# Kernel optimization log

Hardware: AMD Instinct MI355X
Metric: run time of the kernel (lower is better)

Reference implementation:

```python
import jax, jax.numpy as jnp
import numpy as np

N = 20000      # nodes
E = 160000     # edges (avg degree 16)
IN_DIM = 256
HID = 128      # hidden_dim == per-head out_channels in PyG TransformerConv
HEADS = 4
EPS = 1e-5


def setup_inputs() -> dict:
    key = jax.random.key(0)
    ks = jax.random.split(key, 24)

    def w(k, shape, scale=0.05):
        return jax.random.normal(k, shape, dtype=jnp.float32) * scale

    inp = {
        "x": jax.random.normal(ks[0], (N, IN_DIM), dtype=jnp.float32),
        "edge_index": jax.random.randint(ks[1], (2, E), 0, N, dtype=jnp.int32),
        # input projection
        "lin_w": w(ks[2], (IN_DIM, HID)), "lin_b": jnp.zeros((HID,), jnp.float32),
    }
    i = 3
    for l in (1, 2):
        inp[f"q_w{l}"] = w(ks[i], (HID, HEADS * HID)); i += 1
        inp[f"q_b{l}"] = jnp.zeros((HEADS * HID,), jnp.float32)
        inp[f"k_w{l}"] = w(ks[i], (HID, HEADS * HID)); i += 1
        inp[f"k_b{l}"] = jnp.zeros((HEADS * HID,), jnp.float32)
        inp[f"v_w{l}"] = w(ks[i], (HID, HEADS * HID)); i += 1
        inp[f"v_b{l}"] = jnp.zeros((HEADS * HID,), jnp.float32)
        inp[f"s_w{l}"] = w(ks[i], (HID, HID)); i += 1
        inp[f"s_b{l}"] = jnp.zeros((HID,), jnp.float32)
        inp[f"ln_g{l}"] = jnp.ones((HID,), jnp.float32)
        inp[f"ln_b{l}"] = jnp.zeros((HID,), jnp.float32)
    return inp


def _segment_softmax(scores, seg, num):
    # scores: [E, HEADS], seg: [E] destination indices
    m = jax.ops.segment_max(scores, seg, num_segments=num)
    m = jnp.where(jnp.isfinite(m), m, 0.0)  # guard empty segments
    e = jnp.exp(scores - m[seg])
    d = jax.ops.segment_sum(e, seg, num_segments=num)
    return e / (d[seg] + 1e-16)


def _transformer_conv(x, src, dst, qw, qb, kw, kb, vw, vb, sw, sb):
    # PyG TransformerConv(HID, HID, heads=HEADS, concat=False)
    n = x.shape[0]
    q = (x @ qw + qb).reshape(n, HEADS, HID)
    k = (x @ kw + kb).reshape(n, HEADS, HID)
    v = (x @ vw + vb).reshape(n, HEADS, HID)
    # per-edge attention: query at dst (i), key/value at src (j)
    alpha = jnp.einsum("ehd,ehd->eh", q[dst], k[src]) / jnp.sqrt(jnp.float32(HID))
    alpha = _segment_softmax(alpha, dst, n)                 # [E, HEADS]
    msg = v[src] * alpha[..., None]                          # [E, HEADS, HID]
    out = jax.ops.segment_sum(msg, dst, num_segments=n)      # [N, HEADS, HID]
    out = out.mean(axis=1)                                   # concat=False -> head mean
    return out + x @ sw + sb                                 # root skip connection


def _layer_norm(x, g, b):
    mu = x.mean(-1, keepdims=True)
    var = ((x - mu) ** 2).mean(-1, keepdims=True)
    return (x - mu) * jax.lax.rsqrt(var + EPS) * g + b


def reference(x, edge_index, lin_w, lin_b,
              q_w1, q_b1, k_w1, k_b1, v_w1, v_b1, s_w1, s_b1, ln_g1, ln_b1,
              q_w2, q_b2, k_w2, k_b2, v_w2, v_b2, s_w2, s_b2, ln_g2, ln_b2):
    src, dst = edge_index[0], edge_index[1]
    h = jax.nn.relu(x @ lin_w + lin_b)
    h1 = _transformer_conv(h, src, dst, q_w1, q_b1, k_w1, k_b1, v_w1, v_b1, s_w1, s_b1)
    h = _layer_norm(h1 + h, ln_g1, ln_b1)
    h2 = _transformer_conv(h, src, dst, q_w2, q_b2, k_w2, k_b2, v_w2, v_b2, s_w2, s_b2)
    h = _layer_norm(h2 + h, ln_g2, ln_b2)
    return h
```

## Files before the change

### kernel.cpp

```cpp
#include <hip/hip_runtime.h>
#include <math.h>

#define NNODE 20000
#define NEDGE 160000
#define IN_DIMV 256
#define HIDV 128
#define DEGCAP 64
#define BAT 4

typedef __attribute__((ext_vector_type(8))) short bf16x8;
typedef __attribute__((ext_vector_type(4))) float f32x4;
typedef __attribute__((ext_vector_type(2))) float f32x2;

__device__ __forceinline__ float bf2f(unsigned short u) {
    union { unsigned int i; float f; } x; x.i = ((unsigned int)u) << 16; return x.f;
}
__device__ __forceinline__ unsigned short f2bf(float f) {
    union { float f; unsigned int i; } x; x.f = f;
    unsigned int r = x.i + 0x7fffu + ((x.i >> 16) & 1u);
    return (unsigned short)(r >> 16);
}
__device__ __forceinline__ void unpack8(uint4 p, float* f) {
    f[0] = bf2f((unsigned short)(p.x & 0xffff)); f[1] = bf2f((unsigned short)(p.x >> 16));
    f[2] = bf2f((unsigned short)(p.y & 0xffff)); f[3] = bf2f((unsigned short)(p.y >> 16));
    f[4] = bf2f((unsigned short)(p.z & 0xffff)); f[5] = bf2f((unsigned short)(p.z >> 16));
    f[6] = bf2f((unsigned short)(p.w & 0xffff)); f[7] = bf2f((unsigned short)(p.w >> 16));
}
__device__ __forceinline__ void unpack8f8_w(unsigned int a, unsigned int b, float* f) {
    f32x2 t;
    t = __builtin_amdgcn_cvt_pk_f32_fp8((int)a, false); f[0] = t.x; f[1] = t.y;
    t = __builtin_amdgcn_cvt_pk_f32_fp8((int)a, true);  f[2] = t.x; f[3] = t.y;
    t = __builtin_amdgcn_cvt_pk_f32_fp8((int)b, false); f[4] = t.x; f[5] = t.y;
    t = __builtin_amdgcn_cvt_pk_f32_fp8((int)b, true);  f[6] = t.x; f[7] = t.y;
}
__device__ __forceinline__ unsigned char f2fp8(float v) {
    int pk = __builtin_amdgcn_cvt_pk_fp8_f32(v, v, 0, false);
    return (unsigned char)(pk & 0xff);
}
__device__ __forceinline__ void gld_lds16(const unsigned short* g, unsigned short* l) {
    __builtin_amdgcn_global_load_lds((const __attribute__((address_space(1))) void*)g,
                                     (__attribute__((address_space(3))) void*)l, 16, 0, 0);
}

__global__ void convert_kernel(
    const float* __restrict__ lin_w,
    const float* __restrict__ qw0, const float* __restrict__ kw0,
    const float* __restrict__ vw0, const float* __restrict__ sw0,
    const float* __restrict__ qw1, const float* __restrict__ kw1,
    const float* __restrict__ vw1, const float* __restrict__ sw1,
    unsigned short* __restrict__ arena, int* __restrict__ cursor)
{
    int idx = blockIdx.x * 256 + threadIdx.x;
    if (idx < NNODE) cursor[idx] = 0;
    int id2 = idx - NNODE;
    if (id2 < 0 || id2 >= 458752) return;
    float v;
    if (id2 < 32768) {
        int n = id2 >> 8, k = id2 & 255;
        v = lin_w[k * 128 + n];
    } else {
        int t = id2 - 32768;
        int l = t / 212992, r = t % 212992;
        int n = r >> 7, k = r & 127;
        const float* qw = l ? qw1 : qw0;
        const float* kw = l ? kw1 : kw0;
        const float* vw = l ? vw1 : vw0;
        const float* sw = l ? sw1 : sw0;
        if (n < 1536) {
            const float* w = (n < 512) ? qw : (n < 1024) ? kw : vw;
            v = w[k * 512 + (n & 511)];
        } else {
            v = sw[k * 128 + (n - 1536)];
        }
    }
    arena[id2] = f2bf(v);
}

__global__ __launch_bounds__(256) void mfma_gemm0(
    const float* __restrict__ A, const unsigned short* __restrict__ WT,
    const float* __restrict__ b0, unsigned short* __restrict__ hbf_out)
{
    __shared__ unsigned short smem[8192];
    unsigned short* As = smem;
    unsigned short* Bs = smem + 2048;
    unsigned short* ot = smem;
    const int K = 256;

    int tid = threadIdx.x;
    int lane = tid & 63;
    int w = tid >> 6;
    int bm = blockIdx.x * 64;

    int r0 = tid >> 2;
    int c0 = (tid & 3) * 8;
    int g0 = bm + r0; if (g0 > NNODE - 1) g0 = NNODE - 1;
    int srow = lane >> 2;
    int scol = (lane & 3) * 8;
    int sr0 = w * 32 + srow;
    int sr1 = w * 32 + 16 + srow;

    f32x4 acc[4][2] = {};
    int arow = lane & 15;
    int koff = (lane >> 4) * 8;

    for (int k0 = 0; k0 < K; k0 += 32) {
        {
            const float4* p0 = (const float4*)(A + (size_t)g0 * K + k0 + c0);
            float4 u = p0[0], v = p0[1];
            unsigned short t0[8] = {f2bf(u.x), f2bf(u.y), f2bf(u.z), f2bf(u.w),
                                    f2bf(v.x), f2bf(v.y), f2bf(v.z), f2bf(v.w)};
            *(uint4*)&As[r0 * 32 + c0] = *(uint4*)t0;
        }
        gld_lds16(WT + (size_t)sr0 * K + k0 + scol, Bs + sr0 * 32);
        gld_lds16(WT + (size_t)sr1 * K + k0 + scol, Bs + sr1 * 32);
        __syncthreads();
        bf16x8 fa[4], fb[2];
#pragma unroll
        for (int i = 0; i < 4; i++) fa[i] = *(const bf16x8*)&As[(arow + i * 16) * 32 + koff];
#pragma unroll
        for (int i = 0; i < 2; i++) fb[i] = *(const bf16x8*)&Bs[(w * 32 + i * 16 + arow) * 32 + koff];
#pragma unroll
        for (int mi = 0; mi < 4; mi++)
#pragma unroll
            for (int ni = 0; ni < 2; ni++)
                acc[mi][ni] = __builtin_amdgcn_mfma_f32_16x16x32_bf16(fa[mi], fb[ni], acc[mi][ni], 0, 0, 0);
        __syncthreads();
    }

    int quad = lane >> 4, lcol = lane & 15;
#pragma unroll
    for (int mi = 0; mi < 4; mi++) {
#pragma unroll
        for (int ni = 0; ni < 2; ni++) {
            int lc = w * 32 + ni * 16 + lcol;
            float bias = b0[lc];
#pragma unroll
            for (int reg = 0; reg < 4; reg++) {
                float v = fmaxf(acc[mi][ni][reg] + bias, 0.f);
                ot[(mi * 16 + quad * 4 + reg) * 128 + lc] = f2bf(v);
            }
        }
    }
    __syncthreads();
    int r = tid >> 2, q = tid & 3;
    int row = bm + r;
    if (row < NNODE) {
        uint4* dp = (uint4*)(hbf_out + (size_t)row * HIDV + q * 32);
        const uint4* sp = (const uint4*)(ot + r * 128 + q * 32);
#pragma unroll
        for (int qq = 0; qq < 4; qq++) dp[qq] = sp[qq];
    }
}

__global__ __launch_bounds__(256) void mfma_gemm1(
    const unsigned short* __restrict__ A, const unsigned short* __restrict__ WT,
    const float* __restrict__ b0, const float* __restrict__ b1,
    const float* __restrict__ b2, const float* __restrict__ b3,
    unsigned short* __restrict__ qb_out, unsigned char* __restrict__ kv8_out,
    unsigned short* __restrict__ pre16_out)
{
    __shared__ unsigned short As[8192];
    __shared__ unsigned short Ws[16384];
    unsigned short* ot = Ws;
    unsigned char* ot8 = (unsigned char*)Ws;
    const int K = 128;

    int tid = threadIdx.x;
    int lane = tid & 63;
    int w = tid >> 6;
    int bm = blockIdx.x * 64;
    int p0 = (blockIdx.y == 0) ? 0 : 7;
    int p1 = (blockIdx.y == 0) ? 7 : 13;

    int srow = lane >> 2;
    int scol = (lane & 3) * 8;
    int asr = w * 16 + srow;
    int aar = bm + asr; if (aar > NNODE - 1) aar = NNODE - 1;
    int sr0 = w * 32 + srow;
    int sr1 = w * 32 + 16 + srow;

#pragma unroll
    for (int c = 0; c < 4; c++) {
        gld_lds16(A + (size_t)aar * K + c * 32 + scol, As + c * 2048 + asr * 32);
    }

    int arow = lane & 15;
    int koff = (lane >> 4) * 8;
    int quad = lane >> 4, lcol = lane & 15;

    for (int p = p0; p < p1; p++) {
        int bn = p * 128;
#pragma unroll
        for (int c = 0; c < 4; c++) {
            gld_lds16(WT + (size_t)(bn + sr0) * K + c * 32 + scol, Ws + c * 4096 + sr0 * 32);
            gld_lds16(WT + (size_t)(bn + sr1) * K + c * 32 + scol, Ws + c * 4096 + sr1 * 32);
        }
        __syncthreads();

        f32x4 acc[4][2] = {};
#pragma unroll
        for (int c = 0; c < 4; c++) {
            bf16x8 fa[4], fb[2];
#pragma unroll
            for (int i = 0; i < 4; i++) fa[i] = *(const bf16x8*)&As[c * 2048 + (arow + i * 16) * 32 + koff];
#pragma unroll
            for (int i = 0; i < 2; i++) fb[i] = *(const bf16x8*)&Ws[c * 4096 + (w * 32 + i * 16 + arow) * 32 + koff];
#pragma unroll
            for (int mi = 0; mi < 4; mi++)
#pragma unroll
                for (int ni = 0; ni < 2; ni++)
                    acc[mi][ni] = __builtin_amdgcn_mfma_f32_16x16x32_bf16(fa[mi], fb[ni], acc[mi][ni], 0, 0, 0);
        }
        __syncthreads();

        if (p < 4 || p == 12) {
            const float* bb = (p < 4) ? (b0 + bn) : b3;
#pragma unroll
            for (int mi = 0; mi < 4; mi++) {
#pragma unroll
                for (int ni = 0; ni < 2; ni++) {
                    int lc = w * 32 + ni * 16 + lcol;
                    float bias = bb[lc];
#pragma unroll
                    for (int reg = 0; reg < 4; reg++)
                        ot[(mi * 16 + quad * 4 + reg) * 128 + lc] = f2bf(acc[mi][ni][reg] + bias);
                }
            }
            __syncthreads();
            int r = tid >> 2, q = tid & 3;
            int row = bm + r;
            if (row < NNODE) {
                unsigned short* dst = (p < 4) ? (qb_out + (size_t)row * 512 + bn + q * 32)
                                              : (pre16_out + (size_t)row * HIDV + q * 32);
                const uint4* sp = (const uint4*)(ot + r * 128 + q * 32);
                uint4* dp = (uint4*)dst;
#pragma unroll
                for (int qq = 0; qq < 4; qq++) dp[qq] = sp[qq];
            }
            __syncthreads();
        } else {
            const float* bb = (bn < 1024) ? (b1 + bn - 512) : (b2 + bn - 1024);
            int coff = bn - 512;
#pragma unroll
            for (int mi = 0; mi < 4; mi++) {
#pragma unroll
                for (int ni = 0; ni < 2; ni++) {
                    int lc = w * 32 + ni * 16 + lcol;
                    float bias = bb[lc];
#pragma unroll
                    for (int reg = 0; reg < 4; reg++)
                        ot8[(mi * 16 + quad * 4 + reg) * 128 + lc] = f2fp8(acc[mi][ni][reg] + bias);
                }
            }
            __syncthreads();
            int r = tid >> 2, q = tid & 3;
            int row = bm + r;
            if (row < NNODE) {
                uint4* dp = (uint4*)(kv8_out + (size_t)row * 1024 + coff + q * 32);
                const uint4* sp = (const uint4*)(ot8 + r * 128 + q * 32);
                dp[0] = sp[0]; dp[1] = sp[1];
            }
            __syncthreads();
        }
    }
}

__global__ void scatter_kernel(const int* __restrict__ ei, int* __restrict__ cursor,
                               int* __restrict__ bucket) {
    int e = blockIdx.x * blockDim.x + threadIdx.x;
    if (e < NEDGE) {
        int d = ei[NEDGE + e];
        int slot = atomicAdd(&cursor[d], 1);
        if (slot < DEGCAP) bucket[d * DEGCAP + slot] = ei[e];
    }
}

__global__ __launch_bounds__(256) void attn_ln_kernel(
    const unsigned short* __restrict__ qb, const unsigned char* __restrict__ kv8,
    const int* __restrict__ cursor, const int* __restrict__ bucket,
    const unsigned short* __restrict__ pre16, const float* __restrict__ g,
    const float* __restrict__ b,
    unsigned short* __restrict__ hbf ,
    float* __restrict__ extout)
{
    int lane = threadIdx.x & 63;
    int wid = threadIdx.x >> 6;
    int i = blockIdx.x * 4 + wid;
    int myidx = bucket[i * DEGCAP + lane];
    int cnt = cursor[i]; if (cnt > DEGCAP) cnt = DEGCAP;

    int hg = lane >> 4;
    int sl = lane & 15;
    int off = hg * 128 + sl * 8;

    size_t base = (size_t)i * HIDV + sl * 8;
    uint4 pv_raw = *(const uint4*)(pre16 + base);
    uint4 hv_raw = *(const uint4*)(hbf + base);

    float qr[8];
    {
        uint4 p = *(const uint4*)(qb + (size_t)i * 512 + lane * 8);
        unpack8(p, qr);
#pragma unroll
        for (int j = 0; j < 8; j++) qr[j] *= 0.0883883476483184f;
    }

    float m = -INFINITY, l = 0.f;
    float acc[8] = {0.f, 0.f, 0.f, 0.f, 0.f, 0.f, 0.f, 0.f};

    if (cnt > 0) {
        uint2 kA[BAT], vA[BAT], kB[BAT], vB[BAT];

        auto issue = [&](uint2 (&KB)[BAT], uint2 (&VB)[BAT], int bb) {
#pragma unroll
            for (int t = 0; t < BAT; t++) {
                int j = bb * BAT + t; if (j >= cnt) j = cnt - 1;
                int src = __shfl(myidx, j);
                const unsigned char* bp = kv8 + (size_t)src * 1024 + off;
                KB[t] = *(const uint2*)bp;
                VB[t] = *(const uint2*)(bp + 512);
            }
        };

        auto consume = [&](const uint2 (&KB)[BAT], const uint2 (&VB)[BAT], int bb) {
            int rem = cnt - bb * BAT;
            float d[BAT];
#pragma unroll
            for (int t = 0; t < BAT; t++) d[t] = -3.0e38f;
#pragma unroll
            for (int t = 0; t < BAT; t++) {
                if (t >= rem) break;
                float kf[8];
                unpack8f8_w(KB[t].x, KB[t].y, kf);
                d[t] = qr[0] * kf[0] + qr[1] * kf[1] + qr[2] * kf[2] + qr[3] * kf[3] +
                       qr[4] * kf[4] + qr[5] * kf[5] + qr[6] * kf[6] + qr[7] * kf[7];
            }
#pragma unroll
            for (int t = 0; t < BAT; t++) { if (t >= rem) break; d[t] += __shfl_xor(d[t], 8); }
#pragma unroll
            for (int t = 0; t < BAT; t++) { if (t >= rem) break; d[t] += __shfl_xor(d[t], 4); }
#pragma unroll
            for (int t = 0; t < BAT; t++) { if (t >= rem) break; d[t] += __shfl_xor(d[t], 2); }
#pragma unroll
            for (int t = 0; t < BAT; t++) { if (t >= rem) break; d[t] += __shfl_xor(d[t], 1); }

            float mq = d[0];
#pragma unroll
            for (int t = 1; t < BAT; t++) mq = fmaxf(mq, d[t]);
            float mn = fmaxf(m, mq);
            float scale = __expf(m - mn);
            float p[BAT];
            float psum = 0.f;
#pragma unroll
            for (int t = 0; t < BAT; t++) { p[t] = __expf(d[t] - mn); psum += p[t]; }
            l = l * scale + psum;
            m = mn;
#pragma unroll
            for (int c = 0; c < 8; c++) acc[c] *= scale;
#pragma unroll
            for (int t = 0; t < BAT; t++) {
                if (t >= rem) break;
                float vf[8];
                unpack8f8_w(VB[t].x, VB[t].y, vf);
                float pt = p[t];
#pragma unroll
                for (int c = 0; c < 8; c++) acc[c] += pt * vf[c];
            }
        };

        int nb = (cnt + BAT - 1) >> 2;
        issue(kA, vA, 0);
        for (int bb = 0; bb < nb; bb += 2) {
            if (bb + 1 < nb) issue(kB, vB, bb + 1);
            consume(kA, vA, bb);
            if (bb + 1 < nb) {
                if (bb + 2 < nb) issue(kA, vA, bb + 2);
                consume(kB, vB, bb + 1);
            }
        }
    }

    float linv = 0.25f / (l + 1e-16f);
#pragma unroll
    for (int c = 0; c < 8; c++) acc[c] *= linv;
#pragma unroll
    for (int c = 0; c < 8; c++) {
        acc[c] += __shfl_xor(acc[c], 16);
        acc[c] += __shfl_xor(acc[c], 32);
    }

    float pv[8], hv[8];
    unpack8(pv_raw, pv);
    unpack8(hv_raw, hv);
    float vals[8];
#pragma unroll
    for (int c = 0; c < 8; c++) vals[c] = acc[c] + pv[c] + hv[c];

    float s = 0.f;
#pragma unroll
    for (int c = 0; c < 8; c++) s += vals[c];
    s += __shfl_xor(s, 1); s += __shfl_xor(s, 2);
    s += __shfl_xor(s, 4); s += __shfl_xor(s, 8);
    float mu = s * (1.f / 128.f);
    float vs = 0.f;
#pragma unroll
    for (int c = 0; c < 8; c++) { float dx = vals[c] - mu; vs += dx * dx; }
    vs += __shfl_xor(vs, 1); vs += __shfl_xor(vs, 2);
    vs += __shfl_xor(vs, 4); vs += __shfl_xor(vs, 8);
    float rstd = rsqrtf(vs * (1.f / 128.f) + 1e-5f);

    float4 g0 = ((const float4*)(g + sl * 8))[0];
    float4 g1 = ((const float4*)(g + sl * 8))[1];
    float4 bb0 = ((const float4*)(b + sl * 8))[0];
    float4 bb1 = ((const float4*)(b + sl * 8))[1];
    float y[8];
    y[0] = (vals[0] - mu) * rstd * g0.x + bb0.x; y[1] = (vals[1] - mu) * rstd * g0.y + bb0.y;
    y[2] = (vals[2] - mu) * rstd * g0.z + bb0.z; y[3] = (vals[3] - mu) * rstd * g0.w + bb0.w;
    y[4] = (vals[4] - mu) * rstd * g1.x + bb1.x; y[5] = (vals[5] - mu) * rstd * g1.y + bb1.y;
    y[6] = (vals[6] - mu) * rstd * g1.z + bb1.z; y[7] = (vals[7] - mu) * rstd * g1.w + bb1.w;

    if (lane < 16) {
        unsigned short tmp[8] = {f2bf(y[0]), f2bf(y[1]), f2bf(y[2]), f2bf(y[3]),
                                 f2bf(y[4]), f2bf(y[5]), f2bf(y[6]), f2bf(y[7])};
        *(uint4*)(hbf + base) = *(uint4*)tmp;
        if (extout) {
            ((float4*)(extout + base))[0] = make_float4(y[0], y[1], y[2], y[3]);
            ((float4*)(extout + base))[1] = make_float4(y[4], y[5], y[6], y[7]);
        }
    }
}

extern "C" void kernel_launch(void* const* d_in, const int* in_sizes, int n_in,
                              void* d_out, int out_size, void* d_ws, size_t ws_size,
                              hipStream_t stream) {
    const float* x = (const float*)d_in[0];
    const int* ei = (const int*)d_in[1];

    char* ws = (char*)d_ws;
    unsigned short* hbf = (unsigned short*)(ws + 0);
    unsigned short* pre16 = (unsigned short*)(ws + 5120000);
    unsigned short* qb = (unsigned short*)(ws + 10240000);
    unsigned char* kv8 = (unsigned char*)(ws + 30720000);
    int* cursor = (int*)(ws + 51200000);
    int* bucket = (int*)(ws + 51280000);
    unsigned short* arena = (unsigned short*)(ws + 56400000);

    convert_kernel<<<(NNODE + 458752 + 255) / 256, 256, 0, stream>>>(
        (const float*)d_in[2],
        (const float*)d_in[4], (const float*)d_in[6], (const float*)d_in[8], (const float*)d_in[10],
        (const float*)d_in[14], (const float*)d_in[16], (const float*)d_in[18], (const float*)d_in[20],
        arena, cursor);

    scatter_kernel<<<(NEDGE + 255) / 256, 256, 0, stream>>>(ei, cursor, bucket);

    const int GM64 = (NNODE + 63) / 64;

    mfma_gemm0<<<GM64, 256, 0, stream>>>(x, arena, (const float*)d_in[3], hbf);

    for (int l = 0; l < 2; l++) {
        int o = 4 + l * 10;
        const unsigned short* WT = arena + 32768 + l * 212992;
        mfma_gemm1<<<dim3(GM64, 2), 256, 0, stream>>>(
            hbf, WT,
            (const float*)d_in[o + 1], (const float*)d_in[o + 3],
            (const float*)d_in[o + 5], (const float*)d_in[o + 7],
            qb, kv8, pre16);

        attn_ln_kernel<<<NNODE / 4, 256, 0, stream>>>(
            qb, kv8, cursor, bucket, pre16,
            (const float*)d_in[o + 8], (const float*)d_in[o + 9],
            hbf, (l == 1) ? (float*)d_out : nullptr);
    }
}
```

Before: 266.2 us.

## Fuse edge scatter and layer weight conversion into gemm0 as auxiliary blocks

Splits the weight-conversion kernel so only lin_w conversion and cursor reset run first. The edge bucketing scatter and the per-layer QKV/skip weight conversion now run as extra blocks of the first GEMM kernel, so they overlap with it. This drops one launch and the serial dependency chain. The conversion writes are now transposed relative to the reads, which may change memory coalescing.

```diff
diff --git a/kernel.cpp b/kernel.cpp
--- a/kernel.cpp
+++ b/kernel.cpp
@@ -42,45 +42,69 @@
                                      (__attribute__((address_space(3))) void*)l, 16, 0, 0);
 }
 
-__global__ void convert_kernel(
-    const float* __restrict__ lin_w,
+__global__ void prep_kernel(const float* __restrict__ lin_w,
+                            unsigned short* __restrict__ arena, int* __restrict__ cursor)
+{
+    int idx = blockIdx.x * 256 + threadIdx.x;
+    if (idx < NNODE) cursor[idx] = 0;
+    int t = idx - NNODE;
+    if (t < 0 || t >= 32768) return;
+    int k = t >> 7;
+    int n = t & 127;
+    arena[n * 256 + k] = f2bf(lin_w[k * 128 + n]);
+}
+
+__global__ __launch_bounds__(256) void gemm0_fused(
+    const float* __restrict__ A, const unsigned short* __restrict__ WT,
+    const float* __restrict__ b0, unsigned short* __restrict__ hbf_out,
     const float* __restrict__ qw0, const float* __restrict__ kw0,
     const float* __restrict__ vw0, const float* __restrict__ sw0,
     const float* __restrict__ qw1, const float* __restrict__ kw1,
     const float* __restrict__ vw1, const float* __restrict__ sw1,
-    unsigned short* __restrict__ arena, int* __restrict__ cursor)
-{
-    int idx = blockIdx.x * 256 + threadIdx.x;
-    if (idx < NNODE) cursor[idx] = 0;
-    int id2 = idx - NNODE;
-    if (id2 < 0 || id2 >= 458752) return;
-    float v;
-    if (id2 < 32768) {
-        int n = id2 >> 8, k = id2 & 255;
-        v = lin_w[k * 128 + n];
-    } else {
-        int t = id2 - 32768;
-        int l = t / 212992, r = t % 212992;
-        int n = r >> 7, k = r & 127;
-        const float* qw = l ? qw1 : qw0;
-        const float* kw = l ? kw1 : kw0;
-        const float* vw = l ? vw1 : vw0;
-        const float* sw = l ? sw1 : sw0;
-        if (n < 1536) {
-            const float* w = (n < 512) ? qw : (n < 1024) ? kw : vw;
-            v = w[k * 512 + (n & 511)];
-        } else {
-            v = sw[k * 128 + (n - 1536)];
-        }
-    }
-    arena[id2] = f2bf(v);
-}
-
-__global__ __launch_bounds__(256) void mfma_gemm0(
-    const float* __restrict__ A, const unsigned short* __restrict__ WT,
-    const float* __restrict__ b0, unsigned short* __restrict__ hbf_out)
+    const int* __restrict__ ei, int* __restrict__ cursor, int* __restrict__ bucket,
+    unsigned short* __restrict__ arena_big)
 {
     __shared__ unsigned short smem[8192];
+
+    if (blockIdx.x >= 313) {
+        int aux = (blockIdx.x - 313) * 256 + threadIdx.x;
+        {
+            int e = aux;
+            if (e < NEDGE) {
+                int d = ei[NEDGE + e];
+                int slot = atomicAdd(&cursor[d], 1);
+                if (slot < DEGCAP) bucket[d * DEGCAP + slot] = ei[e];
+            }
+            e = aux + 106496;
+            if (e < NEDGE) {
+                int d = ei[NEDGE + e];
+                int slot = atomicAdd(&cursor[d], 1);
+                if (slot < DEGCAP) bucket[d * DEGCAP + slot] = ei[e];
+            }
+        }
+#pragma unroll
+        for (int pass = 0; pass < 4; pass++) {
+            int t2 = aux + pass * 106496;
+            int l = t2 / 212992;
+            int r = t2 % 212992;
+            int k = r / 1664;
+            int n = r % 1664;
+            const float* qw = l ? qw1 : qw0;
+            const float* kw = l ? kw1 : kw0;
+            const float* vw = l ? vw1 : vw0;
+            const float* sw = l ? sw1 : sw0;
+            float v;
+            if (n < 1536) {
+                const float* w = (n < 512) ? qw : (n < 1024) ? kw : vw;
+                v = w[k * 512 + (n & 511)];
+            } else {
+                v = sw[k * 128 + (n - 1536)];
+            }
+            arena_big[l * 212992 + n * 128 + k] = f2bf(v);
+        }
+        return;
+    }
+
     unsigned short* As = smem;
     unsigned short* Bs = smem + 2048;
     unsigned short* ot = smem;
@@ -262,16 +286,6 @@
             }
             __syncthreads();
         }
-    }
-}
-
-__global__ void scatter_kernel(const int* __restrict__ ei, int* __restrict__ cursor,
-                               int* __restrict__ bucket) {
-    int e = blockIdx.x * blockDim.x + threadIdx.x;
-    if (e < NEDGE) {
-        int d = ei[NEDGE + e];
-        int slot = atomicAdd(&cursor[d], 1);
-        if (slot < DEGCAP) bucket[d * DEGCAP + slot] = ei[e];
     }
 }
 
@@ -445,17 +459,16 @@
     int* bucket = (int*)(ws + 51280000);
     unsigned short* arena = (unsigned short*)(ws + 56400000);
 
-    convert_kernel<<<(NNODE + 458752 + 255) / 256, 256, 0, stream>>>(
-        (const float*)d_in[2],
+    prep_kernel<<<(NNODE + 32768 + 255) / 256, 256, 0, stream>>>(
+        (const float*)d_in[2], arena, cursor);
+
+    const int GM64 = (NNODE + 63) / 64;
+
+    gemm0_fused<<<GM64 + 416, 256, 0, stream>>>(
+        x, arena, (const float*)d_in[3], hbf,
         (const float*)d_in[4], (const float*)d_in[6], (const float*)d_in[8], (const float*)d_in[10],
         (const float*)d_in[14], (const float*)d_in[16], (const float*)d_in[18], (const float*)d_in[20],
-        arena, cursor);
-
-    scatter_kernel<<<(NEDGE + 255) / 256, 256, 0, stream>>>(ei, cursor, bucket);
-
-    const int GM64 = (NNODE + 63) / 64;
-
-    mfma_gemm0<<<GM64, 256, 0, stream>>>(x, arena, (const float*)d_in[3], hbf);
+        ei, cursor, bucket, arena + 32768);
 
     for (int l = 0; l < 2; l++) {
         int o = 4 + l * 10;
```

Measured after the change: 261.0 us. Within noise of the previous version (-2.0%).
